# Kernel optimization log

Measured on AMD Instinct MI355X. Metric: run time of the kernel, lower is better.

Reference implementation:

```python
import jax, jax.numpy as jnp
import numpy as np

B, E, NH = 32, 4096, 32
D = E // NH            # head_dim = 128
MAX_TOKENS = 2048
MAX_POS = 1536         # next_pos values in [0, MAX_POS); max pinned so max_k is static


def setup_inputs() -> dict:
    key = jax.random.key(0)
    k0, k1, k2, k3, k4, k5 = jax.random.split(key, 6)
    x = jax.random.normal(k0, (B, 1, E), jnp.float32)
    next_pos = jax.random.randint(k1, (B,), 0, MAX_POS, jnp.int32)
    next_pos = next_pos.at[0].set(MAX_POS - 1)  # pin max so sliced cache length is fixed
    scale = 0.02
    Wq = jax.random.normal(k2, (D, E), jnp.float32) * scale
    Wk = jax.random.normal(k3, (D, E), jnp.float32) * scale
    Wv = jax.random.normal(k4, (D, E), jnp.float32) * scale
    kv_cache = jax.random.normal(k5, (2, B, MAX_TOKENS, D), jnp.float32) * scale
    return {"x": x, "Wq": Wq, "Wk": Wk, "Wv": Wv, "kv_cache": kv_cache, "next_pos": next_pos}


def reference(x, Wq, Wk, Wv, kv_cache, next_pos):
    # x: (B, 1, E); torch Linear(y = x @ W.T)
    q = jnp.einsum('bse,de->bsd', x, Wq)  # (B,1,D)
    k = jnp.einsum('bse,de->bsd', x, Wk)
    v = jnp.einsum('bse,de->bsd', x, Wv)

    # scatter the new step into the cache at each sequence's next_pos
    bidx = jnp.arange(x.shape[0])
    kv = kv_cache.at[0, bidx, next_pos].set(k[:, 0])
    kv = kv.at[1, bidx, next_pos].set(v[:, 0])

    next_pos_new = next_pos + 1
    max_k = int(jax.device_get(jnp.max(next_pos_new)))  # static given pinned next_pos

    k_cache = kv[0, :, :max_k]  # (B, max_k, D)
    v_cache = kv[1, :, :max_k]

    scores = jnp.einsum('bsd,btd->bst', q, k_cache) * (D ** -0.5)  # (B,1,max_k)
    # Faithful to torch: (max_k,max_k) tril mask broadcasts scores to (B,max_k,max_k)
    tril = jnp.tril(jnp.ones((max_k, max_k), dtype=bool))
    masked = jnp.where(tril[None], scores, -jnp.inf)  # (B, max_k, max_k)
    attn = jax.nn.softmax(masked, axis=-1)
    out = attn @ v_cache  # (B, max_k, D)
    return out
```

## Files before the change

### kernel.cpp

```cpp
#include <hip/hip_runtime.h>
#include <math.h>

#define CHUNK 32
#define MAXNC 128

__global__ void proj_kernel(const float* __restrict__ x,
                            const float* __restrict__ Wq,
                            const float* __restrict__ Wk,
                            const float* __restrict__ Wv,
                            float* __restrict__ qkv,
                            int B, int E, int D)
{
    int d = blockIdx.x;
    int b = blockIdx.y;
    int lane = threadIdx.x;
    const float* xrow = x + (size_t)b * E;
    size_t woff = (size_t)d * E;
    float aq = 0.f, ak = 0.f, av = 0.f;
    for (int i = lane * 4; i < E; i += 64 * 4) {
        float4 x4 = *(const float4*)(xrow + i);
        float4 q4 = *(const float4*)(Wq + woff + i);
        float4 k4 = *(const float4*)(Wk + woff + i);
        float4 v4 = *(const float4*)(Wv + woff + i);
        aq += x4.x*q4.x + x4.y*q4.y + x4.z*q4.z + x4.w*q4.w;
        ak += x4.x*k4.x + x4.y*k4.y + x4.z*k4.z + x4.w*k4.w;
        av += x4.x*v4.x + x4.y*v4.y + x4.z*v4.z + x4.w*v4.w;
    }
    #pragma unroll
    for (int off = 32; off >= 1; off >>= 1) {
        aq += __shfl_xor(aq, off, 64);
        ak += __shfl_xor(ak, off, 64);
        av += __shfl_xor(av, off, 64);
    }
    if (lane == 0) {
        qkv[(size_t)b * D + d] = aq;
        qkv[((size_t)B + b) * D + d] = ak;
        qkv[((size_t)2 * B + b) * D + d] = av;
    }
}

__global__ void score_chunk_kernel(const float* __restrict__ kv,
                                   const float* __restrict__ qkv,
                                   const int* __restrict__ next_pos,
                                   float* __restrict__ s_out,
                                   float* __restrict__ m_out,
                                   float* __restrict__ l_out,
                                   float* __restrict__ acc_out,
                                   int B, int D, int T, int MT, int NC, float scale)
{
    int c = blockIdx.x;
    int b = blockIdx.y;
    int tid = threadIdx.x;
    int wave = tid >> 6;
    int lane = tid & 63;
    int l16 = lane & 15;
    int g16 = lane >> 4;

    __shared__ float s_sh[CHUNK];
    __shared__ float w_sh[CHUNK];
    __shared__ float part[8][128];

    int np = next_pos[b];
    int t0 = c * CHUNK;
    const float* q    = qkv + (size_t)b * D;
    const float* knew = qkv + ((size_t)B + b) * D;
    const float* kbase = kv + (size_t)b * MT * D;
    const float4* vnew4 = (const float4*)(qkv + ((size_t)2 * B + b) * D);
    const float4* vbase4 = (const float4*)(kv + ((size_t)B + b) * MT * D);

    float4 qa = *(const float4*)(q + l16 * 8);
    float4 qb = *(const float4*)(q + l16 * 8 + 4);

    #pragma unroll
    for (int p = 0; p < 2; ++p) {
        int j = wave * 8 + p * 4 + g16;
        int t = t0 + j;
        const float* krow = (t == np) ? knew : (kbase + (size_t)t * D);
        float4 ka = *(const float4*)(krow + l16 * 8);
        float4 kb = *(const float4*)(krow + l16 * 8 + 4);
        float ps = qa.x*ka.x + qa.y*ka.y + qa.z*ka.z + qa.w*ka.w
                 + qb.x*kb.x + qb.y*kb.y + qb.z*kb.z + qb.w*kb.w;
        ps += __shfl_xor(ps, 1, 64);
        ps += __shfl_xor(ps, 2, 64);
        ps += __shfl_xor(ps, 4, 64);
        ps += __shfl_xor(ps, 8, 64);
        if (l16 == 0) {
            float sv = (t < T) ? ps * scale : -1e30f;
            s_sh[j] = sv;
            if (t < T) s_out[(size_t)b * T + t] = sv;
        }
    }
    __syncthreads();

    if (wave == 0) {
        float sv = s_sh[lane & 31];
        float m = sv;
        #pragma unroll
        for (int off = 16; off >= 1; off >>= 1)
            m = fmaxf(m, __shfl_xor(m, off, 64));
        float w = __expf(sv - m);
        w_sh[lane & 31] = w;
        float l = w;
        #pragma unroll
        for (int off = 16; off >= 1; off >>= 1)
            l += __shfl_xor(l, off, 64);
        if (lane == 0) {
            m_out[(size_t)b * NC + c] = m;
            l_out[(size_t)b * NC + c] = l;
        }
    }
    __syncthreads();

    int rg = tid >> 5;
    int d4 = tid & 31;
    float4 a4 = make_float4(0.f, 0.f, 0.f, 0.f);
    #pragma unroll
    for (int p = 0; p < 4; ++p) {
        int j = rg * 4 + p;
        int t = t0 + j;
        float4 vv = (t == np) ? vnew4[d4] : vbase4[(size_t)t * 32 + d4];
        float w = w_sh[j];
        a4.x += w * vv.x; a4.y += w * vv.y; a4.z += w * vv.z; a4.w += w * vv.w;
    }
    ((float4*)&part[rg][d4 * 4])[0] = a4;
    __syncthreads();
    if (tid < 128) {
        float s = 0.f;
        #pragma unroll
        for (int r = 0; r < 8; ++r) s += part[r][tid];
        acc_out[((size_t)b * NC + c) * D + tid] = s;
    }
}

__global__ void scan_kernel(const float* __restrict__ m_in,
                            const float* __restrict__ l_in,
                            const float* __restrict__ acc_in,
                            float* __restrict__ Mc_out,
                            float* __restrict__ carryL_out,
                            float* __restrict__ carryA_out,
                            int B, int D, int NC)
{
    int b = blockIdx.x;
    int tid = threadIdx.x;

    extern __shared__ float sh[];
    float* accs = sh;
    float* m_l  = sh + (size_t)NC * 128;
    float* l_l  = m_l + NC;

    const float4* asrc = (const float4*)(acc_in + (size_t)b * NC * D);
    float4* adst = (float4*)accs;
    for (int i = tid; i < NC * 32; i += 128)
        adst[i] = asrc[i];
    if (tid < NC) {
        m_l[tid] = m_in[(size_t)b * NC + tid];
        l_l[tid] = l_in[(size_t)b * NC + tid];
    }
    __syncthreads();

    float M = -1e30f, A = 0.f, L = 0.f;
    float* caout = carryA_out + (size_t)b * NC * D + tid;
    for (int c = 0; c < NC; ++c) {
        float mc = m_l[c];
        float Mn = fmaxf(M, mc);
        float e_old = __expf(M - Mn);
        float Ac = A * e_old;
        caout[(size_t)c * D] = Ac;
        if (tid == 0) {
            Mc_out[(size_t)b * NC + c] = Mn;
            carryL_out[(size_t)b * NC + c] = L * e_old;
        }
        float e_c = __expf(mc - Mn);
        A = Ac + e_c * accs[c * 128 + tid];
        L = L * e_old + e_c * l_l[c];
        M = Mn;
    }
}

__global__ void out_kernel(const float* __restrict__ kv,
                           const float* __restrict__ qkv,
                           const int* __restrict__ next_pos,
                           const float* __restrict__ s_in,
                           const float* __restrict__ Mc_in,
                           const float* __restrict__ carryL_in,
                           const float* __restrict__ carryA_in,
                           float* __restrict__ out,
                           int B, int D, int T, int MT, int NC)
{
    int c = blockIdx.x;
    int b = blockIdx.y;
    int tid = threadIdx.x;

    __shared__ float vs[CHUNK * 128];
    __shared__ float w_sh[CHUNK];
    __shared__ float rl_sh[CHUNK];

    int np = next_pos[b];
    int t0 = c * CHUNK;
    float M = Mc_in[(size_t)b * NC + c];

    const float4* vnew4 = (const float4*)(qkv + ((size_t)2 * B + b) * D);
    const float4* vbase4 = (const float4*)(kv + ((size_t)B + b) * MT * D);

    float A = 0.f;
    if (tid < 128) {
        A = carryA_in[((size_t)b * NC + c) * D + tid];
        if (tid < CHUNK) {
            int t = t0 + tid;
            w_sh[tid] = (t < T) ? __expf(s_in[(size_t)b * T + t] - M) : 0.f;
        }
    } else {
        int t2 = tid - 128;
        #pragma unroll
        for (int r = 0; r < 8; ++r) {
            int i4 = t2 + r * 128;
            int j = i4 >> 5;
            int t = t0 + j;
            float4 vv = (t == np) ? vnew4[i4 & 31]
                                  : vbase4[(size_t)t * 32 + (i4 & 31)];
            ((float4*)vs)[i4] = vv;
        }
    }
    __syncthreads();

    if (tid < CHUNK) {
        float L = carryL_in[(size_t)b * NC + c];
        for (int r = 0; r <= tid; ++r)
            L += w_sh[r];
        rl_sh[tid] = 1.0f / L;
    }
    __syncthreads();

    if (tid < 128) {
        float* orow = out + ((size_t)b * T + t0) * (size_t)D + tid;
        #pragma unroll
        for (int j = 0; j < CHUNK; ++j) {
            int t = t0 + j;
            if (t >= T) break;
            A += w_sh[j] * vs[j * 128 + tid];
            orow[(size_t)j * D] = A * rl_sh[j];
        }
    }
}

extern "C" void kernel_launch(void* const* d_in, const int* in_sizes, int n_in,
                              void* d_out, int out_size, void* d_ws, size_t ws_size,
                              hipStream_t stream) {
    const float* x        = (const float*)d_in[0];
    const float* Wq       = (const float*)d_in[1];
    const float* Wk       = (const float*)d_in[2];
    const float* Wv       = (const float*)d_in[3];
    const float* kv       = (const float*)d_in[4];
    const int*   next_pos = (const int*)d_in[5];
    float* out = (float*)d_out;

    const int B  = in_sizes[5];
    const int E  = in_sizes[0] / B;
    const int D  = in_sizes[1] / E;
    const int T  = out_size / (B * D);
    const int MT = in_sizes[4] / (2 * B * D);
    const int NC = (T + CHUNK - 1) / CHUNK;

    float* ws     = (float*)d_ws;
    float* qkv    = ws;
    float* s      = qkv + (size_t)3 * B * D;
    float* m      = s + (size_t)B * T;
    float* l      = m + (size_t)B * NC;
    float* acc    = l + (size_t)B * NC;
    float* Mc     = acc + (size_t)B * NC * D;
    float* carryL = Mc + (size_t)B * NC;
    float* carryA = carryL + (size_t)B * NC;

    const float scale = 1.0f / sqrtf((float)D);

    proj_kernel<<<dim3(D, B), 64, 0, stream>>>(x, Wq, Wk, Wv, qkv, B, E, D);
    score_chunk_kernel<<<dim3(NC, B), 256, 0, stream>>>(kv, qkv, next_pos,
                                                        s, m, l, acc,
                                                        B, D, T, MT, NC, scale);
    size_t scan_lds = ((size_t)NC * 128 + 2 * NC) * sizeof(float);
    scan_kernel<<<dim3(B), 128, scan_lds, stream>>>(m, l, acc, Mc, carryL, carryA,
                                                    B, D, NC);
    out_kernel<<<dim3(NC, B), 256, 0, stream>>>(kv, qkv, next_pos,
                                                s, Mc, carryL, carryA, out,
                                                B, D, T, MT, NC);
}
```

Baseline: 134.7 us.

## Fuse chunk prefix scan into output kernel and share weight loads across batch pairs

Removes the separate sequential scan kernel: each output block now recomputes the online-softmax prefix over all preceding chunk summaries itself, which drops one launch and the carry-array round trip through global memory. The cost is redundant work that grows with chunk index (up to NC=48 steps, each reading a 128-float acc row), and it makes later blocks longer. The projection kernel also processes two batch rows per block so each weight row is loaded once for two rows, halving weight reads.

```diff
diff --git a/kernel.cpp b/kernel.cpp
--- a/kernel.cpp
+++ b/kernel.cpp
@@ -2,7 +2,6 @@
 #include <math.h>
 
 #define CHUNK 32
-#define MAXNC 128
 
 __global__ void proj_kernel(const float* __restrict__ x,
                             const float* __restrict__ Wq,
@@ -11,31 +10,47 @@
                             float* __restrict__ qkv,
                             int B, int E, int D)
 {
-    int d = blockIdx.x;
-    int b = blockIdx.y;
+    int d  = blockIdx.x;
+    int b0 = blockIdx.y * 2;
+    int b1 = b0 + 1;
+    bool has_b1 = (b1 < B);
     int lane = threadIdx.x;
-    const float* xrow = x + (size_t)b * E;
+    const float* x0 = x + (size_t)b0 * E;
+    const float* x1 = x + (size_t)(has_b1 ? b1 : b0) * E;
     size_t woff = (size_t)d * E;
-    float aq = 0.f, ak = 0.f, av = 0.f;
+    float aq0 = 0.f, ak0 = 0.f, av0 = 0.f;
+    float aq1 = 0.f, ak1 = 0.f, av1 = 0.f;
     for (int i = lane * 4; i < E; i += 64 * 4) {
-        float4 x4 = *(const float4*)(xrow + i);
         float4 q4 = *(const float4*)(Wq + woff + i);
         float4 k4 = *(const float4*)(Wk + woff + i);
         float4 v4 = *(const float4*)(Wv + woff + i);
-        aq += x4.x*q4.x + x4.y*q4.y + x4.z*q4.z + x4.w*q4.w;
-        ak += x4.x*k4.x + x4.y*k4.y + x4.z*k4.z + x4.w*k4.w;
-        av += x4.x*v4.x + x4.y*v4.y + x4.z*v4.z + x4.w*v4.w;
+        float4 xa = *(const float4*)(x0 + i);
+        float4 xb = *(const float4*)(x1 + i);
+        aq0 += xa.x*q4.x + xa.y*q4.y + xa.z*q4.z + xa.w*q4.w;
+        ak0 += xa.x*k4.x + xa.y*k4.y + xa.z*k4.z + xa.w*k4.w;
+        av0 += xa.x*v4.x + xa.y*v4.y + xa.z*v4.z + xa.w*v4.w;
+        aq1 += xb.x*q4.x + xb.y*q4.y + xb.z*q4.z + xb.w*q4.w;
+        ak1 += xb.x*k4.x + xb.y*k4.y + xb.z*k4.z + xb.w*k4.w;
+        av1 += xb.x*v4.x + xb.y*v4.y + xb.z*v4.z + xb.w*v4.w;
     }
     #pragma unroll
     for (int off = 32; off >= 1; off >>= 1) {
-        aq += __shfl_xor(aq, off, 64);
-        ak += __shfl_xor(ak, off, 64);
-        av += __shfl_xor(av, off, 64);
+        aq0 += __shfl_xor(aq0, off, 64);
+        ak0 += __shfl_xor(ak0, off, 64);
+        av0 += __shfl_xor(av0, off, 64);
+        aq1 += __shfl_xor(aq1, off, 64);
+        ak1 += __shfl_xor(ak1, off, 64);
+        av1 += __shfl_xor(av1, off, 64);
     }
     if (lane == 0) {
-        qkv[(size_t)b * D + d] = aq;
-        qkv[((size_t)B + b) * D + d] = ak;
-        qkv[((size_t)2 * B + b) * D + d] = av;
+        qkv[(size_t)b0 * D + d] = aq0;
+        qkv[((size_t)B + b0) * D + d] = ak0;
+        qkv[((size_t)2 * B + b0) * D + d] = av0;
+        if (has_b1) {
+            qkv[(size_t)b1 * D + d] = aq1;
+            qkv[((size_t)B + b1) * D + d] = ak1;
+            qkv[((size_t)2 * B + b1) * D + d] = av1;
+        }
     }
 }
 
@@ -132,58 +147,13 @@
     }
 }
 
-__global__ void scan_kernel(const float* __restrict__ m_in,
-                            const float* __restrict__ l_in,
-                            const float* __restrict__ acc_in,
-                            float* __restrict__ Mc_out,
-                            float* __restrict__ carryL_out,
-                            float* __restrict__ carryA_out,
-                            int B, int D, int NC)
-{
-    int b = blockIdx.x;
-    int tid = threadIdx.x;
-
-    extern __shared__ float sh[];
-    float* accs = sh;
-    float* m_l  = sh + (size_t)NC * 128;
-    float* l_l  = m_l + NC;
-
-    const float4* asrc = (const float4*)(acc_in + (size_t)b * NC * D);
-    float4* adst = (float4*)accs;
-    for (int i = tid; i < NC * 32; i += 128)
-        adst[i] = asrc[i];
-    if (tid < NC) {
-        m_l[tid] = m_in[(size_t)b * NC + tid];
-        l_l[tid] = l_in[(size_t)b * NC + tid];
-    }
-    __syncthreads();
-
-    float M = -1e30f, A = 0.f, L = 0.f;
-    float* caout = carryA_out + (size_t)b * NC * D + tid;
-    for (int c = 0; c < NC; ++c) {
-        float mc = m_l[c];
-        float Mn = fmaxf(M, mc);
-        float e_old = __expf(M - Mn);
-        float Ac = A * e_old;
-        caout[(size_t)c * D] = Ac;
-        if (tid == 0) {
-            Mc_out[(size_t)b * NC + c] = Mn;
-            carryL_out[(size_t)b * NC + c] = L * e_old;
-        }
-        float e_c = __expf(mc - Mn);
-        A = Ac + e_c * accs[c * 128 + tid];
-        L = L * e_old + e_c * l_l[c];
-        M = Mn;
-    }
-}
-
 __global__ void out_kernel(const float* __restrict__ kv,
                            const float* __restrict__ qkv,
                            const int* __restrict__ next_pos,
                            const float* __restrict__ s_in,
-                           const float* __restrict__ Mc_in,
-                           const float* __restrict__ carryL_in,
-                           const float* __restrict__ carryA_in,
+                           const float* __restrict__ m_in,
+                           const float* __restrict__ l_in,
+                           const float* __restrict__ acc_in,
                            float* __restrict__ out,
                            int B, int D, int T, int MT, int NC)
 {
@@ -197,14 +167,28 @@
 
     int np = next_pos[b];
     int t0 = c * CHUNK;
-    float M = Mc_in[(size_t)b * NC + c];
 
     const float4* vnew4 = (const float4*)(qkv + ((size_t)2 * B + b) * D);
     const float4* vbase4 = (const float4*)(kv + ((size_t)B + b) * MT * D);
 
-    float A = 0.f;
+    float A = 0.f, L = 0.f, M = -1e30f;
     if (tid < 128) {
-        A = carryA_in[((size_t)b * NC + c) * D + tid];
+        const float* mrow = m_in + (size_t)b * NC;
+        const float* lrow = l_in + (size_t)b * NC;
+        const float* arow = acc_in + ((size_t)b * NC) * D + tid;
+        for (int cc = 0; cc < c; ++cc) {
+            float mc = mrow[cc];
+            float Mn = fmaxf(M, mc);
+            float eo = __expf(M - Mn);
+            float ec = __expf(mc - Mn);
+            A = A * eo + ec * arow[(size_t)cc * D];
+            L = L * eo + ec * lrow[cc];
+            M = Mn;
+        }
+        float mc = mrow[c];
+        float Mn = fmaxf(M, mc);
+        float eo = __expf(M - Mn);
+        A *= eo; L *= eo; M = Mn;
         if (tid < CHUNK) {
             int t = t0 + tid;
             w_sh[tid] = (t < T) ? __expf(s_in[(size_t)b * T + t] - M) : 0.f;
@@ -224,10 +208,10 @@
     __syncthreads();
 
     if (tid < CHUNK) {
-        float L = carryL_in[(size_t)b * NC + c];
+        float Lr = L;
         for (int r = 0; r <= tid; ++r)
-            L += w_sh[r];
-        rl_sh[tid] = 1.0f / L;
+            Lr += w_sh[r];
+        rl_sh[tid] = 1.0f / Lr;
     }
     __syncthreads();
 
@@ -261,26 +245,20 @@
     const int MT = in_sizes[4] / (2 * B * D);
     const int NC = (T + CHUNK - 1) / CHUNK;
 
-    float* ws     = (float*)d_ws;
-    float* qkv    = ws;
-    float* s      = qkv + (size_t)3 * B * D;
-    float* m      = s + (size_t)B * T;
-    float* l      = m + (size_t)B * NC;
-    float* acc    = l + (size_t)B * NC;
-    float* Mc     = acc + (size_t)B * NC * D;
-    float* carryL = Mc + (size_t)B * NC;
-    float* carryA = carryL + (size_t)B * NC;
+    float* ws  = (float*)d_ws;
+    float* qkv = ws;
+    float* s   = qkv + (size_t)3 * B * D;
+    float* m   = s + (size_t)B * T;
+    float* l   = m + (size_t)B * NC;
+    float* acc = l + (size_t)B * NC;
 
     const float scale = 1.0f / sqrtf((float)D);
 
-    proj_kernel<<<dim3(D, B), 64, 0, stream>>>(x, Wq, Wk, Wv, qkv, B, E, D);
+    proj_kernel<<<dim3(D, (B + 1) / 2), 64, 0, stream>>>(x, Wq, Wk, Wv, qkv, B, E, D);
     score_chunk_kernel<<<dim3(NC, B), 256, 0, stream>>>(kv, qkv, next_pos,
                                                         s, m, l, acc,
                                                         B, D, T, MT, NC, scale);
-    size_t scan_lds = ((size_t)NC * 128 + 2 * NC) * sizeof(float);
-    scan_kernel<<<dim3(B), 128, scan_lds, stream>>>(m, l, acc, Mc, carryL, carryA,
-                                                    B, D, NC);
     out_kernel<<<dim3(NC, B), 256, 0, stream>>>(kv, qkv, next_pos,
-                                                s, Mc, carryL, carryA, out,
+                                                s, m, l, acc, out,
                                                 B, D, T, MT, NC);
 }
```

Result: no change. 136.8 us (+1.5%).
